# Kernel tuning notes

Measured on AMD Instinct MI355X. Metric: run time of the kernel, lower is better.

Reference implementation:

```python
import jax, jax.numpy as jnp
import numpy as np
from jax import lax

B, CM, CQ, CO, H, W, KS = 8, 64, 64, 64, 128, 128, 3
K = KS * KS  # 9 kernel taps, offset_group=1


def setup_inputs() -> dict:
    key = jax.random.key(0)
    k1, k2, k3, k4 = jax.random.split(key, 4)
    mem = jax.random.normal(k1, (B, CM, H, W), jnp.float32)
    que = jax.random.normal(k2, (B, CQ, H, W), jnp.float32)
    # conv_offset: Conv2d(CM+CQ -> 3*K, 3x3, pad=1, bias=True); small init so offsets are a few px
    w_off = jax.random.normal(k3, (3 * K, CM + CQ, KS, KS), jnp.float32) * 0.01
    b_off = jnp.zeros((3 * K,), jnp.float32)
    # deformable conv weight: [CO, CM, 3, 3], bias=False
    w_def = jax.random.normal(k4, (CO, CM, KS, KS), jnp.float32) * (1.0 / np.sqrt(CM * K))
    return {"mem": mem, "que": que, "w_off": w_off, "b_off": b_off, "w_def": w_def}


def _deform_conv2d(mem, offset, mask, w_def):
    """Deformable conv v2 (stride=1, pad=1, dil=1, groups=1, offset_group=1).
    mem: [B,C,H,W]; offset: [B,2K,H,W] (dy,dx pairs per tap); mask: [B,K,H,W]."""
    Bn, C, Hn, Wn = mem.shape
    Kn = w_def.shape[2] * w_def.shape[3]
    off = offset.reshape(Bn, Kn, 2, Hn, Wn)
    dy, dx = off[:, :, 0], off[:, :, 1]            # [B,K,H,W]
    kk = jnp.arange(Kn)
    ky = (kk // KS - 1).astype(jnp.float32)        # kernel tap offsets with pad=1, dil=1
    kx = (kk % KS - 1).astype(jnp.float32)
    gy = jnp.arange(Hn, dtype=jnp.float32)
    gx = jnp.arange(Wn, dtype=jnp.float32)
    py = gy[None, None, :, None] + ky[None, :, None, None] + dy   # sample y coords [B,K,H,W]
    px = gx[None, None, None, :] + kx[None, :, None, None] + dx   # sample x coords [B,K,H,W]
    y0 = jnp.floor(py)
    x0 = jnp.floor(px)
    fy = py - y0
    fx = px - x0
    b_idx = jnp.arange(Bn)[:, None, None, None]

    def corner(iy, ix, wgt):
        valid = (iy >= 0) & (iy < Hn) & (ix >= 0) & (ix < Wn)  # zero padding outside
        iyc = jnp.clip(iy.astype(jnp.int32), 0, Hn - 1)
        ixc = jnp.clip(ix.astype(jnp.int32), 0, Wn - 1)
        vals = mem[b_idx, :, iyc, ixc]             # gather -> [B,K,H,W,C]
        return vals * (wgt * valid)[..., None]

    sampled = (corner(y0, x0, (1 - fy) * (1 - fx))
               + corner(y0, x0 + 1, (1 - fy) * fx)
               + corner(y0 + 1, x0, fy * (1 - fx))
               + corner(y0 + 1, x0 + 1, fy * fx))
    sampled = sampled * mask[..., None]            # modulation (applied raw, as in source)
    w = w_def.reshape(w_def.shape[0], C, Kn)       # [O,C,K]; tap order kh*KS+kw matches kk
    return jnp.einsum('bkhwc,ock->bohw', sampled, w)


def reference(mem, que, w_off, b_off, w_def):
    x = jnp.concatenate([mem, que], axis=1)
    off = lax.conv_general_dilated(
        x, w_off, window_strides=(1, 1), padding=[(1, 1), (1, 1)],
        dimension_numbers=('NCHW', 'OIHW', 'NCHW')) + b_off[None, :, None, None]
    offset, mask = off[:, :2 * K], off[:, 2 * K:]
    return _deform_conv2d(mem, offset, mask, w_def)
```

## Files before the change

### kernel.cpp

```cpp
#include <hip/hip_runtime.h>
#include <hip/hip_bf16.h>

#define Bn   8
#define CM_  64
#define CIN  128
#define CO_  64
#define Hn   128
#define Wn   128
#define Kn   9
#define COFF 27
#define HW   (Hn * Wn)

typedef __attribute__((ext_vector_type(8))) short bf16x8;
typedef __attribute__((ext_vector_type(4))) float f32x4;
typedef __attribute__((ext_vector_type(2))) float f32x2;

__device__ __forceinline__ unsigned short f2bf(float x) {
    union { float f; unsigned u; } v; v.f = x;
    unsigned r = v.u + 0x7FFF + ((v.u >> 16) & 1);
    return (unsigned short)(r >> 16);
}
__device__ __forceinline__ float blo(unsigned u) {
    union { unsigned u; float f; } v; v.u = u << 16; return v.f;
}
__device__ __forceinline__ float bhi(unsigned u) {
    union { unsigned u; float f; } v; v.u = u & 0xffff0000u; return v.f;
}
__device__ __forceinline__ unsigned pack_bf2(float lo, float hi) {
    __hip_bfloat162 r = __float22bfloat162_rn(make_float2(lo, hi));
    unsigned u;
    __builtin_memcpy(&u, &r, 4);
    return u;
}

__global__ __launch_bounds__(256) void transpose_kernel(
    const float* __restrict__ mem, const float* __restrict__ que,
    uint4* __restrict__ xT4)
{
    __shared__ unsigned tile[64 * 65];

    const int bb   = blockIdx.x & 7;
    const int pix0 = (blockIdx.x >> 3) * 64;
    const int tid  = threadIdx.x;
    const int pxL  = tid & 63;
    const int cg   = tid >> 6;

    const float* mb = mem + (size_t)bb * CM_ * HW + pix0 + pxL;
    const float* qb = que + (size_t)bb * CM_ * HW + pix0 + pxL;

    #pragma unroll
    for (int i = 0; i < 16; ++i) {
        const int c = cg * 32 + 2 * i;
        const float v0 = (c < CM_) ? mb[(size_t)c * HW]       : qb[(size_t)(c - CM_) * HW];
        const float v1 = (c + 1 < CM_) ? mb[(size_t)(c + 1) * HW] : qb[(size_t)(c + 1 - CM_) * HW];
        tile[pxL * 65 + cg * 16 + i] =
            (unsigned)f2bf(v0) | ((unsigned)f2bf(v1) << 16);
    }
    __syncthreads();

    uint4* dst = xT4 + (size_t)(bb * HW + pix0) * 16;
    #pragma unroll
    for (int p = 0; p < 4; ++p) {
        const int G  = p * 256 + tid;
        const int px = G >> 4;
        const int u  = G & 15;
        uint4 v;
        v.x = tile[px * 65 + u * 4 + 0];
        v.y = tile[px * 65 + u * 4 + 1];
        v.z = tile[px * 65 + u * 4 + 2];
        v.w = tile[px * 65 + u * 4 + 3];
        dst[G] = v;
    }
}

__global__ __launch_bounds__(256) void wprep_def_kernel(
    const float* __restrict__ w_def, unsigned short* __restrict__ wp)
{
    const int idx = blockIdx.x * 256 + threadIdx.x;
    if (idx >= CO_ * CM_ * Kn) return;
    const int j  = idx & 7;
    const int L  = (idx >> 3) & 63;
    const int f  = (idx >> 9) & 1;
    const int gk = idx >> 10;
    const int k  = gk % 9;
    const int g  = gk / 9;
    const int o  = g * 16 + (L & 15);
    const int c  = f * 32 + (L >> 4) * 8 + j;
    wp[idx] = f2bf(w_def[(size_t)(o * CM_ + c) * Kn + k]);
}

__global__ __launch_bounds__(256) void wprep_off_kernel(
    const float* __restrict__ w_off, unsigned short* __restrict__ wp)
{
    const int idx = blockIdx.x * 256 + threadIdx.x;
    if (idx >= 2 * 9 * 4 * 64 * 8) return;
    const int j   = idx & 7;
    const int L   = (idx >> 3) & 63;
    const int s   = (idx >> 9) & 3;
    const int r   = idx >> 11;
    const int tap = r % 9;
    const int ot  = r / 9;
    const int o   = ot * 16 + (L & 15);
    const int c   = s * 32 + (L >> 4) * 8 + j;
    wp[idx] = (o < COFF) ? f2bf(w_off[(size_t)(o * CIN + c) * Kn + tap]) : (unsigned short)0;
}

__global__ __launch_bounds__(256) void off_conv_mfma(
    const uint4* __restrict__ xT4, const uint4* __restrict__ wpo,
    const float* __restrict__ b_off, float* __restrict__ off)
{
    __shared__ uint4 xw[198 * 16];

    const int bb   = blockIdx.x & 7;
    const int pix0 = (blockIdx.x >> 3) * 64;
    const int h    = pix0 >> 7;
    const int w0   = pix0 & 127;
    const int tid  = threadIdx.x;
    const int wv   = tid >> 6;
    const int lane = tid & 63;
    const int quad = lane >> 4;
    const int lrow = lane & 15;
    const int ot   = wv >> 1;
    const int sub0 = (wv & 1) * 2;

    const uint4* xb = xT4 + (size_t)bb * HW * 16;

    #pragma unroll
    for (int g = 0; g < 13; ++g) {
        const int idx = g * 256 + tid;
        if (idx < 198 * 16) {
            const int slot = idx >> 4;
            const int j    = idx & 15;
            const int r    = slot / 66;
            const int c    = slot - r * 66;
            const int y    = h + r - 1;
            const int x    = w0 + c - 1;
            const bool ok  = (y >= 0) & (y < Hn) & (x >= 0) & (x < Wn);
            uint4 v = make_uint4(0, 0, 0, 0);
            if (ok) v = xb[(size_t)(y * Wn + x) * 16 + j];
            xw[slot * 16 + (j ^ (slot & 7))] = v;
        }
    }
    __syncthreads();

    f32x4 acc[2];
    #pragma unroll
    for (int t = 0; t < 2; ++t)
        #pragma unroll
        for (int r = 0; r < 4; ++r) {
            const int o = ot * 16 + quad * 4 + r;
            acc[t][r] = (o < COFF) ? b_off[o] : 0.0f;
        }

    #pragma unroll
    for (int tap = 0; tap < 9; ++tap) {
        const int rr = tap / 3;
        const int cc = tap % 3;

        const uint4* ap = wpo + (size_t)((ot * 9 + tap) * 4) * 64 + lane;
        bf16x8 a[4];
        #pragma unroll
        for (int s = 0; s < 4; ++s) a[s] = __builtin_bit_cast(bf16x8, ap[s * 64]);

        #pragma unroll
        for (int t = 0; t < 2; ++t) {
            const int pl   = (sub0 + t) * 16 + lrow;
            const int slot = rr * 66 + pl + cc;
            const int base = slot * 16;
            const int sw   = slot & 7;
            #pragma unroll
            for (int s = 0; s < 4; ++s) {
                const bf16x8 bfrag = __builtin_bit_cast(bf16x8,
                    xw[base + ((s * 4 + quad) ^ sw)]);
                acc[t] = __builtin_amdgcn_mfma_f32_16x16x32_bf16(
                    a[s], bfrag, acc[t], 0, 0, 0);
            }
        }
    }

    #pragma unroll
    for (int t = 0; t < 2; ++t) {
        const int pp = pix0 + (sub0 + t) * 16 + lrow;
        #pragma unroll
        for (int r = 0; r < 4; ++r) {
            const int o = ot * 16 + quad * 4 + r;
            if (o < COFF)
                off[(size_t)(bb * COFF + o) * HW + pp] = acc[t][r];
        }
    }
}

__global__ __launch_bounds__(256) void deform_mfma_kernel(
    const uint4* __restrict__ xT4, const float* __restrict__ off,
    const uint4* __restrict__ wprep, float* __restrict__ out)
{
    __shared__ uint4 smp4[2][64 * 8];

    const int bb    = blockIdx.x & 7;
    const int pix0  = (blockIdx.x >> 3) * 64;
    const int tid   = threadIdx.x;
    const int wv    = tid >> 6;
    const int lane  = tid & 63;
    const int quad  = lane >> 4;
    const int lrow  = lane & 15;
    const int chunk = lane & 7;
    const int psub  = lane >> 3;

    const uint4*  xb      = xT4 + (size_t)bb * HW * 16;
    const float*  offbase = off + (size_t)bb * COFF * HW;

    const int pM = pix0 + lane;
    const int hM = pM >> 7;
    const int wM = pM & 127;

    f32x4 acc[4];
    #pragma unroll
    for (int i = 0; i < 4; ++i) acc[i] = (f32x4){0.f, 0.f, 0.f, 0.f};

    float W00[2], W01[2], W10[2], W11[2];
    uint4 G00[2], G01[2], G10[2], G11[2];

    auto prep = [&](int k) {
        const float dy = offbase[(2 * k    ) * HW + pM];
        const float dx = offbase[(2 * k + 1) * HW + pM];
        const float mk = offbase[(18 + k   ) * HW + pM];
        const float py = (float)(hM + k / 3 - 1) + dy;
        const float px = (float)(wM + k % 3 - 1) + dx;
        const float y0f = floorf(py), x0f = floorf(px);
        const float fy = py - y0f,  fx = px - x0f;
        const int y0 = (int)y0f, x0 = (int)x0f;
        const int y1 = y0 + 1,   x1 = x0 + 1;
        const bool vy0 = (y0 >= 0) & (y0 < Hn);
        const bool vy1 = (y1 >= 0) & (y1 < Hn);
        const bool vx0 = (x0 >= 0) & (x0 < Wn);
        const bool vx1 = (x1 >= 0) & (x1 < Wn);
        const float w00 = (1.f - fy) * (1.f - fx) * (float)(vy0 & vx0) * mk;
        const float w01 = (1.f - fy) * fx         * (float)(vy0 & vx1) * mk;
        const float w10 = fy * (1.f - fx)         * (float)(vy1 & vx0) * mk;
        const float w11 = fy * fx                 * (float)(vy1 & vx1) * mk;
        const int y0c = min(max(y0, 0), Hn - 1);
        const int y1c = min(max(y1, 0), Hn - 1);
        const int x0c = min(max(x0, 0), Wn - 1);
        const int x1c = min(max(x1, 0), Wn - 1);
        const int i00 = y0c * Wn + x0c, i01 = y0c * Wn + x1c;
        const int i10 = y1c * Wn + x0c, i11 = y1c * Wn + x1c;

        #pragma unroll
        for (int g = 0; g < 2; ++g) {
            const int pl = g * 32 + wv * 8 + psub;
            W00[g] = __shfl(w00, pl, 64);
            W01[g] = __shfl(w01, pl, 64);
            W10[g] = __shfl(w10, pl, 64);
            W11[g] = __shfl(w11, pl, 64);
            const int I00 = __shfl(i00, pl, 64);
            const int I01 = __shfl(i01, pl, 64);
            const int I10 = __shfl(i10, pl, 64);
            const int I11 = __shfl(i11, pl, 64);
            G00[g] = xb[(size_t)I00 * 16 + chunk];
            G01[g] = xb[(size_t)I01 * 16 + chunk];
            G10[g] = xb[(size_t)I10 * 16 + chunk];
            G11[g] = xb[(size_t)I11 * 16 + chunk];
        }
    };

    auto blendwrite = [&](int buf) {
        #pragma unroll
        for (int g = 0; g < 2; ++g) {
            const int pl = g * 32 + wv * 8 + psub;
            const unsigned u00[4] = {G00[g].x, G00[g].y, G00[g].z, G00[g].w};
            const unsigned u01[4] = {G01[g].x, G01[g].y, G01[g].z, G01[g].w};
            const unsigned u10[4] = {G10[g].x, G10[g].y, G10[g].z, G10[g].w};
            const unsigned u11[4] = {G11[g].x, G11[g].y, G11[g].z, G11[g].w};
            unsigned pk[4];
            #pragma unroll
            for (int d = 0; d < 4; ++d) {
                const f32x2 c00 = {blo(u00[d]), bhi(u00[d])};
                const f32x2 c01 = {blo(u01[d]), bhi(u01[d])};
                const f32x2 c10 = {blo(u10[d]), bhi(u10[d])};
                const f32x2 c11 = {blo(u11[d]), bhi(u11[d])};
                const f32x2 s = W00[g] * c00 + W01[g] * c01
                              + W10[g] * c10 + W11[g] * c11;
                pk[d] = pack_bf2(s.x, s.y);
            }
            smp4[buf][pl * 8 + (chunk ^ (pl & 7))] =
                make_uint4(pk[0], pk[1], pk[2], pk[3]);
        }
    };

    prep(0);
    blendwrite(0);
    __syncthreads();

    #pragma unroll
    for (int k = 0; k < Kn; ++k) {
        const int cur = k & 1;

        if (k < Kn - 1) prep(k + 1);

        const uint4* wpk = wprep + (size_t)((wv * 9 + k) * 2) * 64 + lane;
        const bf16x8 a0 = __builtin_bit_cast(bf16x8, wpk[0]);
        const bf16x8 a1 = __builtin_bit_cast(bf16x8, wpk[64]);

        #pragma unroll
        for (int nt = 0; nt < 4; ++nt) {
            const int pm = nt * 16 + lrow;
            const bf16x8 b0 = __builtin_bit_cast(bf16x8,
                smp4[cur][pm * 8 + ( quad      ^ (pm & 7))]);
            const bf16x8 b1 = __builtin_bit_cast(bf16x8,
                smp4[cur][pm * 8 + ((quad + 4) ^ (pm & 7))]);
            acc[nt] = __builtin_amdgcn_mfma_f32_16x16x32_bf16(a0, b0, acc[nt], 0, 0, 0);
            acc[nt] = __builtin_amdgcn_mfma_f32_16x16x32_bf16(a1, b1, acc[nt], 0, 0, 0);
        }

        if (k < Kn - 1) blendwrite(cur ^ 1);
        __syncthreads();
    }

    const int obase = (wv << 4) + (quad << 2);
    #pragma unroll
    for (int nt = 0; nt < 4; ++nt) {
        const int pp = pix0 + nt * 16 + lrow;
        #pragma unroll
        for (int r = 0; r < 4; ++r)
            out[(size_t)(bb * CO_ + obase + r) * HW + pp] = acc[nt][r];
    }
}

extern "C" void kernel_launch(void* const* d_in, const int* in_sizes, int n_in,
                              void* d_out, int out_size, void* d_ws, size_t ws_size,
                              hipStream_t stream) {
    const float* mem   = (const float*)d_in[0];
    const float* que   = (const float*)d_in[1];
    const float* w_off = (const float*)d_in[2];
    const float* b_off = (const float*)d_in[3];
    const float* w_def = (const float*)d_in[4];
    float* out = (float*)d_out;

    char* ws = (char*)d_ws;
    float*          off  = (float*)ws;
    unsigned short* wpd  = (unsigned short*)(ws + 14155776);
    unsigned short* wpo  = (unsigned short*)(ws + 14229504);
    uint4*          xT4  = (uint4*)(ws + 14303232);

    transpose_kernel<<<2048, 256, 0, stream>>>(mem, que, xT4);
    wprep_def_kernel<<<144, 256, 0, stream>>>(w_def, wpd);
    wprep_off_kernel<<<144, 256, 0, stream>>>(w_off, wpo);
    off_conv_mfma<<<2048, 256, 0, stream>>>(xT4, (const uint4*)wpo, b_off, off);
    deform_mfma_kernel<<<2048, 256, 0, stream>>>(xT4, off, (const uint4*)wpd, out);
}
```

Baseline: 185.9 us.

## Fuse offset conv into deformable conv kernel, switch to fp16 with half2 blending

The offset convolution and the deformable sampling/GEMM now run in one kernel per 64-pixel tile. The offsets and masks stay in LDS instead of going through a global buffer, and one launch is removed. Data and weights move from bf16 to fp16 so bilinear blending can use packed half2 FMA instead of unpacking to fp32. The two weight-prep kernels are merged into one launch. This trades some range and precision (fp16 blend accumulation) and gives LDS occupancy less room for the offset-conv stage.

```diff
diff --git a/kernel.cpp b/kernel.cpp
--- a/kernel.cpp
+++ b/kernel.cpp
@@ -1,5 +1,5 @@
 #include <hip/hip_runtime.h>
-#include <hip/hip_bf16.h>
+#include <hip/hip_fp16.h>
 
 #define Bn   8
 #define CM_  64
@@ -11,26 +11,18 @@
 #define COFF 27
 #define HW   (Hn * Wn)
 
-typedef __attribute__((ext_vector_type(8))) short bf16x8;
+typedef __attribute__((ext_vector_type(8))) _Float16 f16x8;
 typedef __attribute__((ext_vector_type(4))) float f32x4;
-typedef __attribute__((ext_vector_type(2))) float f32x2;
-
-__device__ __forceinline__ unsigned short f2bf(float x) {
-    union { float f; unsigned u; } v; v.f = x;
-    unsigned r = v.u + 0x7FFF + ((v.u >> 16) & 1);
-    return (unsigned short)(r >> 16);
-}
-__device__ __forceinline__ float blo(unsigned u) {
-    union { unsigned u; float f; } v; v.u = u << 16; return v.f;
-}
-__device__ __forceinline__ float bhi(unsigned u) {
-    union { unsigned u; float f; } v; v.u = u & 0xffff0000u; return v.f;
-}
-__device__ __forceinline__ unsigned pack_bf2(float lo, float hi) {
-    __hip_bfloat162 r = __float22bfloat162_rn(make_float2(lo, hi));
-    unsigned u;
-    __builtin_memcpy(&u, &r, 4);
-    return u;
+
+__device__ __forceinline__ unsigned h22u(__half2 h) {
+    unsigned u; __builtin_memcpy(&u, &h, 4); return u;
+}
+__device__ __forceinline__ __half2 u2h2(unsigned u) {
+    __half2 h; __builtin_memcpy(&h, &u, 4); return h;
+}
+__device__ __forceinline__ unsigned short f2h(float x) {
+    __half h = __float2half(x);
+    unsigned short u; __builtin_memcpy(&u, &h, 2); return u;
 }
 
 __global__ __launch_bounds__(256) void transpose_kernel(
@@ -53,8 +45,7 @@
         const int c = cg * 32 + 2 * i;
         const float v0 = (c < CM_) ? mb[(size_t)c * HW]       : qb[(size_t)(c - CM_) * HW];
         const float v1 = (c + 1 < CM_) ? mb[(size_t)(c + 1) * HW] : qb[(size_t)(c + 1 - CM_) * HW];
-        tile[pxL * 65 + cg * 16 + i] =
-            (unsigned)f2bf(v0) | ((unsigned)f2bf(v1) << 16);
+        tile[pxL * 65 + cg * 16 + i] = h22u(__floats2half2_rn(v0, v1));
     }
     __syncthreads();
 
@@ -73,55 +64,57 @@
     }
 }
 
-__global__ __launch_bounds__(256) void wprep_def_kernel(
-    const float* __restrict__ w_def, unsigned short* __restrict__ wp)
+__global__ __launch_bounds__(256) void wprep_all_kernel(
+    const float* __restrict__ w_def, const float* __restrict__ w_off,
+    unsigned short* __restrict__ wpd, unsigned short* __restrict__ wpo)
 {
-    const int idx = blockIdx.x * 256 + threadIdx.x;
-    if (idx >= CO_ * CM_ * Kn) return;
-    const int j  = idx & 7;
-    const int L  = (idx >> 3) & 63;
-    const int f  = (idx >> 9) & 1;
-    const int gk = idx >> 10;
-    const int k  = gk % 9;
-    const int g  = gk / 9;
-    const int o  = g * 16 + (L & 15);
-    const int c  = f * 32 + (L >> 4) * 8 + j;
-    wp[idx] = f2bf(w_def[(size_t)(o * CM_ + c) * Kn + k]);
-}
-
-__global__ __launch_bounds__(256) void wprep_off_kernel(
-    const float* __restrict__ w_off, unsigned short* __restrict__ wp)
+    int idx = blockIdx.x * 256 + threadIdx.x;
+    if (idx < CO_ * CM_ * Kn) {
+        const int j  = idx & 7;
+        const int L  = (idx >> 3) & 63;
+        const int f  = (idx >> 9) & 1;
+        const int gk = idx >> 10;
+        const int k  = gk % 9;
+        const int g  = gk / 9;
+        const int o  = g * 16 + (L & 15);
+        const int c  = f * 32 + (L >> 4) * 8 + j;
+        wpd[idx] = f2h(w_def[(size_t)(o * CM_ + c) * Kn + k]);
+        return;
+    }
+    idx -= CO_ * CM_ * Kn;
+    if (idx < 2 * 9 * 4 * 64 * 8) {
+        const int j   = idx & 7;
+        const int L   = (idx >> 3) & 63;
+        const int s   = (idx >> 9) & 3;
+        const int r   = idx >> 11;
+        const int tap = r % 9;
+        const int ot  = r / 9;
+        const int o   = ot * 16 + (L & 15);
+        const int c   = s * 32 + (L >> 4) * 8 + j;
+        wpo[idx] = (o < COFF) ? f2h(w_off[(size_t)(o * CIN + c) * Kn + tap])
+                              : (unsigned short)0;
+    }
+}
+
+__global__ __launch_bounds__(256) void fused_deform_kernel(
+    const uint4* __restrict__ xT4, const uint4* __restrict__ wpo,
+    const uint4* __restrict__ wpd, const float* __restrict__ b_off,
+    float* __restrict__ out)
 {
-    const int idx = blockIdx.x * 256 + threadIdx.x;
-    if (idx >= 2 * 9 * 4 * 64 * 8) return;
-    const int j   = idx & 7;
-    const int L   = (idx >> 3) & 63;
-    const int s   = (idx >> 9) & 3;
-    const int r   = idx >> 11;
-    const int tap = r % 9;
-    const int ot  = r / 9;
-    const int o   = ot * 16 + (L & 15);
-    const int c   = s * 32 + (L >> 4) * 8 + j;
-    wp[idx] = (o < COFF) ? f2bf(w_off[(size_t)(o * CIN + c) * Kn + tap]) : (unsigned short)0;
-}
-
-__global__ __launch_bounds__(256) void off_conv_mfma(
-    const uint4* __restrict__ xT4, const uint4* __restrict__ wpo,
-    const float* __restrict__ b_off, float* __restrict__ off)
-{
-    __shared__ uint4 xw[198 * 16];
+    __shared__ __align__(16) char lds[198 * 16 * 16];
+    uint4* xw   = (uint4*)lds;
+    float* offl = (float*)lds;
+    uint4* smp4 = (uint4*)(lds + 8192);
 
     const int bb   = blockIdx.x & 7;
     const int pix0 = (blockIdx.x >> 3) * 64;
-    const int h    = pix0 >> 7;
+    const int h0   = pix0 >> 7;
     const int w0   = pix0 & 127;
     const int tid  = threadIdx.x;
     const int wv   = tid >> 6;
     const int lane = tid & 63;
     const int quad = lane >> 4;
     const int lrow = lane & 15;
-    const int ot   = wv >> 1;
-    const int sub0 = (wv & 1) * 2;
 
     const uint4* xb = xT4 + (size_t)bb * HW * 16;
 
@@ -133,7 +126,7 @@
             const int j    = idx & 15;
             const int r    = slot / 66;
             const int c    = slot - r * 66;
-            const int y    = h + r - 1;
+            const int y    = h0 + r - 1;
             const int x    = w0 + c - 1;
             const bool ok  = (y >= 0) & (y < Hn) & (x >= 0) & (x < Wn);
             uint4 v = make_uint4(0, 0, 0, 0);
@@ -143,71 +136,61 @@
     }
     __syncthreads();
 
-    f32x4 acc[2];
-    #pragma unroll
-    for (int t = 0; t < 2; ++t)
-        #pragma unroll
-        for (int r = 0; r < 4; ++r) {
-            const int o = ot * 16 + quad * 4 + r;
-            acc[t][r] = (o < COFF) ? b_off[o] : 0.0f;
-        }
-
-    #pragma unroll
-    for (int tap = 0; tap < 9; ++tap) {
-        const int rr = tap / 3;
-        const int cc = tap % 3;
-
-        const uint4* ap = wpo + (size_t)((ot * 9 + tap) * 4) * 64 + lane;
-        bf16x8 a[4];
-        #pragma unroll
-        for (int s = 0; s < 4; ++s) a[s] = __builtin_bit_cast(bf16x8, ap[s * 64]);
+    {
+        const int ot   = wv >> 1;
+        const int sub0 = (wv & 1) * 2;
+
+        f32x4 oacc[2];
+        #pragma unroll
+        for (int t = 0; t < 2; ++t)
+            #pragma unroll
+            for (int r = 0; r < 4; ++r) {
+                const int o = ot * 16 + quad * 4 + r;
+                oacc[t][r] = (o < COFF) ? b_off[o] : 0.0f;
+            }
+
+        #pragma unroll
+        for (int tap = 0; tap < 9; ++tap) {
+            const int rr = tap / 3;
+            const int cc = tap % 3;
+
+            const uint4* ap = wpo + (size_t)((ot * 9 + tap) * 4) * 64 + lane;
+            f16x8 a[4];
+            #pragma unroll
+            for (int s = 0; s < 4; ++s)
+                a[s] = __builtin_bit_cast(f16x8, ap[s * 64]);
+
+            #pragma unroll
+            for (int t = 0; t < 2; ++t) {
+                const int pl   = (sub0 + t) * 16 + lrow;
+                const int slot = rr * 66 + pl + cc;
+                const int base = slot * 16;
+                const int sw   = slot & 7;
+                #pragma unroll
+                for (int s = 0; s < 4; ++s) {
+                    const f16x8 bfrag = __builtin_bit_cast(f16x8,
+                        xw[base + ((s * 4 + quad) ^ sw)]);
+                    oacc[t] = __builtin_amdgcn_mfma_f32_16x16x32_f16(
+                        a[s], bfrag, oacc[t], 0, 0, 0);
+                }
+            }
+        }
+        __syncthreads();
 
         #pragma unroll
         for (int t = 0; t < 2; ++t) {
-            const int pl   = (sub0 + t) * 16 + lrow;
-            const int slot = rr * 66 + pl + cc;
-            const int base = slot * 16;
-            const int sw   = slot & 7;
-            #pragma unroll
-            for (int s = 0; s < 4; ++s) {
-                const bf16x8 bfrag = __builtin_bit_cast(bf16x8,
-                    xw[base + ((s * 4 + quad) ^ sw)]);
-                acc[t] = __builtin_amdgcn_mfma_f32_16x16x32_bf16(
-                    a[s], bfrag, acc[t], 0, 0, 0);
+            const int pl = (sub0 + t) * 16 + lrow;
+            #pragma unroll
+            for (int r = 0; r < 4; ++r) {
+                const int o = ot * 16 + quad * 4 + r;
+                if (o < COFF) offl[o * 64 + pl] = oacc[t][r];
             }
         }
-    }
-
-    #pragma unroll
-    for (int t = 0; t < 2; ++t) {
-        const int pp = pix0 + (sub0 + t) * 16 + lrow;
-        #pragma unroll
-        for (int r = 0; r < 4; ++r) {
-            const int o = ot * 16 + quad * 4 + r;
-            if (o < COFF)
-                off[(size_t)(bb * COFF + o) * HW + pp] = acc[t][r];
-        }
-    }
-}
-
-__global__ __launch_bounds__(256) void deform_mfma_kernel(
-    const uint4* __restrict__ xT4, const float* __restrict__ off,
-    const uint4* __restrict__ wprep, float* __restrict__ out)
-{
-    __shared__ uint4 smp4[2][64 * 8];
-
-    const int bb    = blockIdx.x & 7;
-    const int pix0  = (blockIdx.x >> 3) * 64;
-    const int tid   = threadIdx.x;
-    const int wv    = tid >> 6;
-    const int lane  = tid & 63;
-    const int quad  = lane >> 4;
-    const int lrow  = lane & 15;
+        __syncthreads();
+    }
+
     const int chunk = lane & 7;
     const int psub  = lane >> 3;
-
-    const uint4*  xb      = xT4 + (size_t)bb * HW * 16;
-    const float*  offbase = off + (size_t)bb * COFF * HW;
 
     const int pM = pix0 + lane;
     const int hM = pM >> 7;
@@ -217,13 +200,13 @@
     #pragma unroll
     for (int i = 0; i < 4; ++i) acc[i] = (f32x4){0.f, 0.f, 0.f, 0.f};
 
-    float W00[2], W01[2], W10[2], W11[2];
-    uint4 G00[2], G01[2], G10[2], G11[2];
+    __half2 W00h[2], W01h[2], W10h[2], W11h[2];
+    uint4   G00[2], G01[2], G10[2], G11[2];
 
     auto prep = [&](int k) {
-        const float dy = offbase[(2 * k    ) * HW + pM];
-        const float dx = offbase[(2 * k + 1) * HW + pM];
-        const float mk = offbase[(18 + k   ) * HW + pM];
+        const float dy = offl[(2 * k    ) * 64 + lane];
+        const float dx = offl[(2 * k + 1) * 64 + lane];
+        const float mk = offl[(18 + k   ) * 64 + lane];
         const float py = (float)(hM + k / 3 - 1) + dy;
         const float px = (float)(wM + k % 3 - 1) + dx;
         const float y0f = floorf(py), x0f = floorf(px);
@@ -248,10 +231,10 @@
         #pragma unroll
         for (int g = 0; g < 2; ++g) {
             const int pl = g * 32 + wv * 8 + psub;
-            W00[g] = __shfl(w00, pl, 64);
-            W01[g] = __shfl(w01, pl, 64);
-            W10[g] = __shfl(w10, pl, 64);
-            W11[g] = __shfl(w11, pl, 64);
+            W00h[g] = __float2half2_rn(__shfl(w00, pl, 64));
+            W01h[g] = __float2half2_rn(__shfl(w01, pl, 64));
+            W10h[g] = __float2half2_rn(__shfl(w10, pl, 64));
+            W11h[g] = __float2half2_rn(__shfl(w11, pl, 64));
             const int I00 = __shfl(i00, pl, 64);
             const int I01 = __shfl(i01, pl, 64);
             const int I10 = __shfl(i10, pl, 64);
@@ -274,15 +257,13 @@
             unsigned pk[4];
             #pragma unroll
             for (int d = 0; d < 4; ++d) {
-                const f32x2 c00 = {blo(u00[d]), bhi(u00[d])};
-                const f32x2 c01 = {blo(u01[d]), bhi(u01[d])};
-                const f32x2 c10 = {blo(u10[d]), bhi(u10[d])};
-                const f32x2 c11 = {blo(u11[d]), bhi(u11[d])};
-                const f32x2 s = W00[g] * c00 + W01[g] * c01
-                              + W10[g] * c10 + W11[g] * c11;
-                pk[d] = pack_bf2(s.x, s.y);
+                __half2 s = __hmul2(u2h2(u00[d]), W00h[g]);
+                s = __hfma2(u2h2(u01[d]), W01h[g], s);
+                s = __hfma2(u2h2(u10[d]), W10h[g], s);
+                s = __hfma2(u2h2(u11[d]), W11h[g], s);
+                pk[d] = h22u(s);
             }
-            smp4[buf][pl * 8 + (chunk ^ (pl & 7))] =
+            smp4[buf * 512 + pl * 8 + (chunk ^ (pl & 7))] =
                 make_uint4(pk[0], pk[1], pk[2], pk[3]);
         }
     };
@@ -297,19 +278,19 @@
 
         if (k < Kn - 1) prep(k + 1);
 
-        const uint4* wpk = wprep + (size_t)((wv * 9 + k) * 2) * 64 + lane;
-        const bf16x8 a0 = __builtin_bit_cast(bf16x8, wpk[0]);
-        const bf16x8 a1 = __builtin_bit_cast(bf16x8, wpk[64]);
+        const uint4* wpk = wpd + (size_t)((wv * 9 + k) * 2) * 64 + lane;
+        const f16x8 a0 = __builtin_bit_cast(f16x8, wpk[0]);
+        const f16x8 a1 = __builtin_bit_cast(f16x8, wpk[64]);
 
         #pragma unroll
         for (int nt = 0; nt < 4; ++nt) {
             const int pm = nt * 16 + lrow;
-            const bf16x8 b0 = __builtin_bit_cast(bf16x8,
-                smp4[cur][pm * 8 + ( quad      ^ (pm & 7))]);
-            const bf16x8 b1 = __builtin_bit_cast(bf16x8,
-                smp4[cur][pm * 8 + ((quad + 4) ^ (pm & 7))]);
-            acc[nt] = __builtin_amdgcn_mfma_f32_16x16x32_bf16(a0, b0, acc[nt], 0, 0, 0);
-            acc[nt] = __builtin_amdgcn_mfma_f32_16x16x32_bf16(a1, b1, acc[nt], 0, 0, 0);
+            const f16x8 b0 = __builtin_bit_cast(f16x8,
+                smp4[cur * 512 + pm * 8 + ( quad      ^ (pm & 7))]);
+            const f16x8 b1 = __builtin_bit_cast(f16x8,
+                smp4[cur * 512 + pm * 8 + ((quad + 4) ^ (pm & 7))]);
+            acc[nt] = __builtin_amdgcn_mfma_f32_16x16x32_f16(a0, b0, acc[nt], 0, 0, 0);
+            acc[nt] = __builtin_amdgcn_mfma_f32_16x16x32_f16(a1, b1, acc[nt], 0, 0, 0);
         }
 
         if (k < Kn - 1) blendwrite(cur ^ 1);
@@ -337,14 +318,12 @@
     float* out = (float*)d_out;
 
     char* ws = (char*)d_ws;
-    float*          off  = (float*)ws;
-    unsigned short* wpd  = (unsigned short*)(ws + 14155776);
-    unsigned short* wpo  = (unsigned short*)(ws + 14229504);
-    uint4*          xT4  = (uint4*)(ws + 14303232);
+    unsigned short* wpd = (unsigned short*)ws;
+    unsigned short* wpo = (unsigned short*)(ws + 73728);
+    uint4*          xT4 = (uint4*)(ws + 147456);
 
     transpose_kernel<<<2048, 256, 0, stream>>>(mem, que, xT4);
-    wprep_def_kernel<<<144, 256, 0, stream>>>(w_def, wpd);
-    wprep_off_kernel<<<144, 256, 0, stream>>>(w_off, wpo);
-    off_conv_mfma<<<2048, 256, 0, stream>>>(xT4, (const uint4*)wpo, b_off, off);
-    deform_mfma_kernel<<<2048, 256, 0, stream>>>(xT4, off, (const uint4*)wpd, out);
-}
+    wprep_all_kernel<<<288, 256, 0, stream>>>(w_def, w_off, wpd, wpo);
+    fused_deform_kernel<<<2048, 256, 0, stream>>>(
+        xT4, (const uint4*)wpo, (const uint4*)wpd, b_off, out);
+}
```

Result: faster. 168.8 us (-9.2%).
